# Kernel tuning notes

Measured on AMD Instinct MI355X. Metric: run time of the kernel, lower is better.

Reference implementation:

```python
import jax, jax.numpy as jnp
import numpy as np


def mp_conv1d(x, w, groups=1, pad=0):
    # EDM2-style magnitude-preserving conv: per-out-channel unit-norm weight, no bias.
    # effective w_hat = w / (eps + ||w||/sqrt(fan_in)) / sqrt(fan_in)  ~= w / ||w||
    fan_in = w.shape[1] * w.shape[2]
    norm = jnp.sqrt(jnp.sum(jnp.square(w), axis=(1, 2), keepdims=True))
    w_hat = w / ((1e-4 + norm / np.sqrt(fan_in)) * np.sqrt(fan_in))
    return jax.lax.conv_general_dilated(
        x, w_hat, window_strides=(1,), padding=[(pad, pad)],
        dimension_numbers=('NCH', 'OIH', 'NCH'), feature_group_count=groups)


def complex_log(x, eps=1e-6):
    real = jnp.log(jnp.maximum(jnp.abs(x), eps))
    imag = (x < 0).astype(real.dtype) * np.pi
    return jax.lax.complex(real, imag)


def logcumsumexp_complex(z, axis=-1):
    # parallel prefix logcumsumexp over complex values (stabilized by real part)
    def combine(a, b):
        m = jnp.maximum(a.real, b.real)
        m_safe = jnp.where(jnp.isfinite(m), m, 0.0)  # guard (-inf,-inf) pairs
        return m_safe + jnp.log(jnp.exp(a - m_safe) + jnp.exp(b - m_safe))
    return jax.lax.associative_scan(combine, z, axis=axis)


def log_parallel_scan(log_a, log_b, log_h0):
    # heinsen associative scan: h[t] = a[t]*h[t-1] + b[t], h[-1]=h0
    log_b = jnp.concatenate([log_h0[..., None].astype(log_b.dtype), log_b], axis=-1)
    pads = [(0, 0)] * (log_a.ndim - 1) + [(1, 0)]
    a_star = jnp.pad(jnp.cumsum(log_a, axis=-1), pads)  # [... L+1]
    log_h0_plus_b_star = logcumsumexp_complex(log_b - a_star, axis=-1)
    log_h = a_star + log_h0_plus_b_star
    return jnp.exp(log_h[..., 1:]).real


def min_gru(h, g):
    # o[t] = (1-sigmoid(g[t])) * o[t-1] + sigmoid(g[t]) * h[t], h0 = 0
    log_a = jax.nn.log_sigmoid(-g)
    log_b = jax.nn.log_sigmoid(g) + complex_log(h)
    log_h0 = jnp.full(h.shape[:-1], -jnp.inf, dtype=log_b.dtype)  # log(0)
    return log_parallel_scan(log_a, log_b, log_h0).astype(h.dtype)


def setup_inputs() -> dict:
    key = jax.random.key(0)
    k1, k2, k3, k4 = jax.random.split(key, 4)
    B, D, L, O = 4, 512, 8192, 512
    return {
        'x': jax.random.normal(k1, (B, D, L), jnp.float32),
        'conv_w': jax.random.normal(k2, (D, 1, 5), jnp.float32),
        'h_w': jax.random.normal(k3, (O, D, 1), jnp.float32),
        'g_w': jax.random.normal(k4, (O - 2, D, 1), jnp.float32),
    }


def reference(x, conv_w, h_w, g_w):
    c = mp_conv1d(x, conv_w, groups=x.shape[1], pad=2)  # depthwise 5-tap
    h = mp_conv1d(c, h_w)                               # [B O L]
    g = mp_conv1d(c, g_w)                               # [B O-2 L]
    B, _, L = g.shape
    g = jnp.concatenate([
        jnp.full((B, 1, L), -1000.0, g.dtype),
        jnp.full((B, 1, L), 1000.0, g.dtype),
        g], axis=1)                                     # polarize -> [B O L]
    return min_gru(h, g)
```

## Files before the change

### kernel.cpp

```cpp
#include <hip/hip_runtime.h>
#include <hip/hip_bf16.h>
#include <math.h>

typedef float f32x4 __attribute__((ext_vector_type(4)));
typedef short s16x8 __attribute__((ext_vector_type(8)));
typedef short s16x16 __attribute__((ext_vector_type(16)));

#define B_  4
#define D_  512
#define L_  8192
#define CH_ 512
#define M_  1024

typedef const __attribute__((address_space(1))) void g_cvoid;
typedef __attribute__((address_space(3))) void lds_void;

__device__ __forceinline__ unsigned short f2bf(float f) {
    union { float f; unsigned u; } v; v.f = f;
    unsigned r = v.u + 0x7FFFu + ((v.u >> 16) & 1u);
    return (unsigned short)(r >> 16);
}

__global__ __launch_bounds__(256)
void prep_kernel(const float* __restrict__ h_w, const float* __restrict__ g_w,
                 unsigned short* __restrict__ Wn) {
    __shared__ float red[4];
    const int ch = blockIdx.x, t = threadIdx.x;
    {
        float v0 = h_w[ch * 512 + t], v1 = h_w[ch * 512 + t + 256];
        float ss = v0 * v0 + v1 * v1;
        #pragma unroll
        for (int off = 32; off > 0; off >>= 1) ss += __shfl_down(ss, off, 64);
        if ((t & 63) == 0) red[t >> 6] = ss;
        __syncthreads();
        float tot = red[0] + red[1] + red[2] + red[3];
        float scale = 1.f / (sqrtf(tot) + 1e-4f * sqrtf(512.f));
        Wn[(size_t)(2 * ch) * 512 + t]       = f2bf(v0 * scale);
        Wn[(size_t)(2 * ch) * 512 + t + 256] = f2bf(v1 * scale);
    }
    __syncthreads();
    if (ch >= 2) {
        float v0 = g_w[(ch - 2) * 512 + t], v1 = g_w[(ch - 2) * 512 + t + 256];
        float ss = v0 * v0 + v1 * v1;
        #pragma unroll
        for (int off = 32; off > 0; off >>= 1) ss += __shfl_down(ss, off, 64);
        if ((t & 63) == 0) red[t >> 6] = ss;
        __syncthreads();
        float tot = red[0] + red[1] + red[2] + red[3];
        float scale = 1.f / (sqrtf(tot) + 1e-4f * sqrtf(512.f));
        Wn[(size_t)(2 * ch + 1) * 512 + t]       = f2bf(v0 * scale);
        Wn[(size_t)(2 * ch + 1) * 512 + t + 256] = f2bf(v1 * scale);
    } else {
        Wn[(size_t)(2 * ch + 1) * 512 + t]       = 0;
        Wn[(size_t)(2 * ch + 1) * 512 + t + 256] = 0;
    }
}

__global__ __launch_bounds__(512)
void w1n_kernel(const float* __restrict__ h_w, float* __restrict__ w1n_g) {
    __shared__ float red[8];
    const int t = threadIdx.x;
    const int sg = t >> 6;
    const int lane = t & 63;
    float v = h_w[512 + t];
    float ss = v * v;
    #pragma unroll
    for (int off = 32; off > 0; off >>= 1) ss += __shfl_down(ss, off, 64);
    if (lane == 0) red[sg] = ss;
    __syncthreads();
    float tot = ((red[0] + red[1]) + (red[2] + red[3]))
              + ((red[4] + red[5]) + (red[6] + red[7]));
    float sc = 1.f / (sqrtf(tot) + 1e-4f * sqrtf(512.f));
    w1n_g[t] = v * sc;
}

__global__ __launch_bounds__(256)
void convT_kernel(const float* __restrict__ x, const float* __restrict__ cw,
                  const float* __restrict__ w1n_g,
                  unsigned short* __restrict__ CT, float* __restrict__ Pp) {
    __shared__ float xs[64][72];
    __shared__ unsigned short ct[64][72];
    __shared__ float cvf[64][65];
    const int t = threadIdx.x;
    const int l0 = blockIdx.x * 64, d0 = blockIdx.y * 64, b = blockIdx.z;
    const int r = t >> 2, q = t & 3;
    const float* xr = x + (size_t)(b * 512 + d0 + r) * L_ + (l0 - 2);
    #pragma unroll
    for (int k = 0; k < 17; ++k) {
        int c = q + 4 * k;
        int lg = l0 - 2 + c;
        xs[r][c] = (lg >= 0 && lg < L_) ? xr[c] : 0.f;
    }
    float w0 = cw[(d0 + r) * 5 + 0], w1 = cw[(d0 + r) * 5 + 1],
          w2 = cw[(d0 + r) * 5 + 2], w3 = cw[(d0 + r) * 5 + 3],
          w4 = cw[(d0 + r) * 5 + 4];
    float ss = w0 * w0 + w1 * w1 + w2 * w2 + w3 * w3 + w4 * w4;
    float scale = 1.f / (sqrtf(ss) + 1e-4f * sqrtf(5.f));
    w0 *= scale; w1 *= scale; w2 *= scale; w3 *= scale; w4 *= scale;
    __syncthreads();
    #pragma unroll
    for (int k = 0; k < 16; ++k) {
        int li = q + 4 * k;
        float acc = w0 * xs[r][li + 0] + w1 * xs[r][li + 1] + w2 * xs[r][li + 2]
                  + w3 * xs[r][li + 3] + w4 * xs[r][li + 4];
        ct[li][r] = f2bf(acc);
        cvf[li][r] = acc;
    }
    __syncthreads();
    {
        int lr = t >> 2, seg = t & 3;
        s16x16 v = *(const s16x16*)&ct[lr][seg * 16];
        *(s16x16*)&CT[(size_t)(b * 8192 + l0 + lr) * 512 + d0 + seg * 16] = v;
    }
    if (t < 64) {
        float p = 0.f;
        for (int rr = 0; rr < 64; ++rr)
            p += w1n_g[d0 + rr] * cvf[t][rr];
        Pp[((size_t)blockIdx.y * B_ + b) * L_ + l0 + t] = p;
    }
}

__global__ __launch_bounds__(256)
void gemm_kernel(const unsigned short* __restrict__ Wn,
                 const unsigned short* __restrict__ CT,
                 unsigned* __restrict__ HG) {
    __shared__ unsigned short As[128 * 64];
    __shared__ unsigned short Bs[128 * 64];
    const int t = threadIdx.x;
    const int lane = t & 63, w = t >> 6;
    const int wgid = ((blockIdx.x & 7) << 8) | (blockIdx.x >> 3);
    const int mBase = (wgid & 7) * 128;
    const int nBase = (wgid >> 3) * 128;

    const int wrow = (w >> 1) * 64, wcol = (w & 1) * 64;

    const int srow_ = lane >> 3;
    const int schk  = (lane & 7) ^ srow_;

    f32x4 acc[4][4];
    #pragma unroll
    for (int fr = 0; fr < 4; ++fr)
        #pragma unroll
        for (int fc = 0; fc < 4; ++fc)
            acc[fr][fc] = (f32x4){0.f, 0.f, 0.f, 0.f};

    const unsigned short* gA = &Wn[(size_t)(mBase + w * 32 + srow_) * 512 + schk * 8];
    const unsigned short* gB = &CT[(size_t)(nBase + w * 32 + srow_) * 512 + schk * 8];

    const int g  = lane >> 4;
    const int c0 = ((0 + g) ^ (lane & 7)) * 8;
    const int c1 = ((4 + g) ^ (lane & 7)) * 8;

    #pragma unroll
    for (int ks = 0; ks < 8; ++ks) {
        const int k0 = ks * 64;
        #pragma unroll
        for (int i = 0; i < 4; ++i) {
            __builtin_amdgcn_global_load_lds(
                (g_cvoid*)(gA + (size_t)i * 8 * 512 + k0),
                (lds_void*)&As[(w * 32 + i * 8) * 64], 16, 0, 0);
            __builtin_amdgcn_global_load_lds(
                (g_cvoid*)(gB + (size_t)i * 8 * 512 + k0),
                (lds_void*)&Bs[(w * 32 + i * 8) * 64], 16, 0, 0);
        }
        __syncthreads();
        #pragma unroll
        for (int kh = 0; kh < 2; ++kh) {
            const int cc = (kh == 0) ? c0 : c1;
            s16x8 af[4], bf[4];
            #pragma unroll
            for (int f = 0; f < 4; ++f) {
                af[f] = *(const s16x8*)&As[(wrow + f * 16 + (lane & 15)) * 64 + cc];
                bf[f] = *(const s16x8*)&Bs[(wcol + f * 16 + (lane & 15)) * 64 + cc];
            }
            #pragma unroll
            for (int fr = 0; fr < 4; ++fr)
                #pragma unroll
                for (int fc = 0; fc < 4; ++fc)
                    acc[fr][fc] = __builtin_amdgcn_mfma_f32_16x16x32_bf16(
                        af[fr], bf[fc], acc[fr][fc], 0, 0, 0);
        }
        __syncthreads();
    }

    #pragma unroll
    for (int fr = 0; fr < 4; ++fr)
    #pragma unroll
    for (int fc = 0; fc < 4; ++fc) {
        f32x4 a = acc[fr][fc];
        const int gR0 = mBase + wrow + fr * 16 + ((lane >> 4) * 4);
        const int n   = nBase + wcol + fc * 16 + (lane & 15);
        const int bb  = n >> 13, l = n & 8191;
        #pragma unroll
        for (int p = 0; p < 2; ++p) {
            float hv = a[2 * p], gv = a[2 * p + 1];
            const int ch = (gR0 >> 1) + p;
            if (ch == 0)      gv = -1000.f;
            else if (ch == 1) gv =  1000.f;
            size_t off = ((size_t)bb * CH_ + ch) * L_ + l;
            HG[off] = ((unsigned)f2bf(hv) << 16) | (unsigned)f2bf(gv);
        }
    }
}

struct LV { float re, sg; };

__device__ __forceinline__ LV lcomb(LV a, LV b) {
    float m  = fmaxf(a.re, b.re);
    float ms = (m > -3.0e38f) ? m : 0.f;
    float s  = a.sg * __expf(a.re - ms) + b.sg * __expf(b.re - ms);
    LV r;
    r.re = ms + __logf(fabsf(s));
    r.sg = (s < 0.f) ? -1.f : 1.f;
    return r;
}

__global__ __launch_bounds__(512)
void logscan_kernel(const unsigned* __restrict__ HG,
                    const float* __restrict__ Pp,
                    float* __restrict__ Out) {
    __shared__ float wA[8];
    __shared__ float wRe[8], wSg[8];
    const int row = blockIdx.x;
    const int t = threadIdx.x;
    const int lane = t & 63, wid = t >> 6;
    const bool isCh1 = ((row & 511) == 1);
    const int bb = row >> 9;
    const unsigned* hp = HG + (size_t)row * L_;
    float* op = Out + (size_t)row * L_;

    float As[16], zz[16];
    unsigned sgb = 0;
    float run = 0.f;
    if (isCh1) {
        #pragma unroll
        for (int i = 0; i < 16; ++i) {
            const int l = t * 16 + i;
            float acc = Pp[((size_t)0 * B_ + bb) * L_ + l];
            #pragma unroll
            for (int gg = 1; gg < 8; ++gg)
                acc += Pp[((size_t)gg * B_ + bb) * L_ + l];
            if (acc < 0.f) sgb |= (1u << i);
            run -= 1000.f;
            As[i] = run;
            zz[i] = logf(fmaxf(fabsf(acc), 1e-6f));
        }
    } else {
        #pragma unroll
        for (int i = 0; i < 4; ++i) {
            uint4 h4 = *(const uint4*)&hp[t * 16 + i * 4];
            #pragma unroll
            for (int j = 0; j < 4; ++j) {
                int k = i * 4 + j;
                unsigned w32 = (j == 0) ? h4.x : (j == 1) ? h4.y
                             : (j == 2) ? h4.z : h4.w;
                float hv = __uint_as_float(w32 & 0xFFFF0000u);
                float gv = __uint_as_float(w32 << 16);
                float e  = __expf(-fabsf(gv));
                float l1 = __logf(1.f + e);
                float la = fminf(-gv, 0.f) - l1;
                float ls = fminf(gv, 0.f) - l1;
                if (hv < 0.f) sgb |= (1u << k);
                run += la;
                As[k] = run;
                zz[k] = ls + __logf(fmaxf(fabsf(hv), 1e-6f));
            }
        }
    }
    float wsc = run;
    #pragma unroll
    for (int off = 1; off < 64; off <<= 1) {
        float u = __shfl_up(wsc, off, 64);
        if (lane >= off) wsc += u;
    }
    if (lane == 63) wA[wid] = wsc;
    __syncthreads();
    float pre = wsc - run;
    for (int j = 0; j < wid; ++j) pre += wA[j];
    #pragma unroll
    for (int i = 0; i < 16; ++i) As[i] += pre;

    LV tot = { -INFINITY, 1.f };
    #pragma unroll
    for (int k = 0; k < 16; ++k) {
        zz[k] -= As[k];
        LV zi = { zz[k], ((sgb >> k) & 1) ? -1.f : 1.f };
        tot = lcomb(tot, zi);
    }
    LV sc = tot;
    #pragma unroll
    for (int off = 1; off < 64; off <<= 1) {
        float ure = __shfl_up(sc.re, off, 64);
        float usg = __shfl_up(sc.sg, off, 64);
        if (lane >= off) { LV u = { ure, usg }; sc = lcomb(u, sc); }
    }
    if (lane == 63) { wRe[wid] = sc.re; wSg[wid] = sc.sg; }
    __syncthreads();
    float pr = __shfl_up(sc.re, 1, 64);
    float ps = __shfl_up(sc.sg, 1, 64);
    LV lex = { -INFINITY, 1.f };
    if (lane != 0) { lex.re = pr; lex.sg = ps; }
    LV wpre = { -INFINITY, 1.f };
    for (int j = 0; j < wid; ++j) { LV u = { wRe[j], wSg[j] }; wpre = lcomb(wpre, u); }
    LV pref = lcomb(wpre, lex);

    LV run2 = pref;
    #pragma unroll
    for (int i = 0; i < 4; ++i) {
        float4 o4;
        #pragma unroll
        for (int j = 0; j < 4; ++j) {
            int k = i * 4 + j;
            LV zi = { zz[k], ((sgb >> k) & 1) ? -1.f : 1.f };
            run2 = lcomb(run2, zi);
            float ov = run2.sg * __expf(As[k] + run2.re);
            if (j == 0) o4.x = ov; else if (j == 1) o4.y = ov;
            else if (j == 2) o4.z = ov; else o4.w = ov;
        }
        *(float4*)&op[t * 16 + i * 4] = o4;
    }
}

extern "C" void kernel_launch(void* const* d_in, const int* in_sizes, int n_in,
                              void* d_out, int out_size, void* d_ws, size_t ws_size,
                              hipStream_t stream) {
    const float* x      = (const float*)d_in[0];
    const float* conv_w = (const float*)d_in[1];
    const float* h_w    = (const float*)d_in[2];
    const float* g_w    = (const float*)d_in[3];
    float* out = (float*)d_out;
    char* ws = (char*)d_ws;

    unsigned short* CT  = (unsigned short*)ws;
    unsigned short* Wn  = (unsigned short*)(ws + (size_t)32 * 1024 * 1024);
    unsigned*       HG  = (unsigned*)(ws + (size_t)33 * 1024 * 1024);
    const size_t base97 = (size_t)97 * 1024 * 1024;
    float* w1n_g = (float*)(ws + base97);
    float* Pp    = (float*)(ws + base97 + 16 * 1024);

    prep_kernel<<<512, 256, 0, stream>>>(h_w, g_w, Wn);
    w1n_kernel<<<1, 512, 0, stream>>>(h_w, w1n_g);
    convT_kernel<<<dim3(128, 8, 4), 256, 0, stream>>>(x, conv_w, w1n_g, CT, Pp);
    gemm_kernel<<<2048, 256, 0, stream>>>(Wn, CT, HG);
    logscan_kernel<<<B_ * CH_, 512, 0, stream>>>(HG, Pp, out);
}
```

Before: 149.5 us.

## Fuse log-sigmoid precompute into GEMM epilogue and simplify local log-scan

The GEMM epilogue now computes the log-sigmoid terms log_a and log_b directly and stores them as two fp16 values packed in one word, replacing the raw bf16 h/g pair. The sign of h is carried in the sign bit of the encoded log_a. The scan kernel therefore does no softplus or log work while loading. Its per-thread reduction and prefix pass also move from repeated pairwise log-add-exp combines to a running max and scaled sum, which removes most per-element log calls. The costs are extra transcendental work in the GEMM epilogue and some precision risk from fp16 storage. There is also an edge case: when log_a rounds to exactly +0, the sign encoding can mark the wrong sign of h.

```diff
diff --git a/kernel.cpp b/kernel.cpp
--- a/kernel.cpp
+++ b/kernel.cpp
@@ -1,5 +1,6 @@
 #include <hip/hip_runtime.h>
 #include <hip/hip_bf16.h>
+#include <hip/hip_fp16.h>
 #include <math.h>
 
 typedef float f32x4 __attribute__((ext_vector_type(4)));
@@ -197,8 +198,16 @@
             const int ch = (gR0 >> 1) + p;
             if (ch == 0)      gv = -1000.f;
             else if (ch == 1) gv =  1000.f;
+            float e  = __expf(-fabsf(gv));
+            float l1 = __logf(1.f + e);
+            float la = fminf(-gv, 0.f) - l1;
+            float ls = fminf(gv, 0.f) - l1;
+            float zb = ls + __logf(fmaxf(fabsf(hv), 1e-6f));
+            float enc = (hv < 0.f) ? -la : la;
+            unsigned short ula = __half_as_ushort(__float2half(enc));
+            unsigned short uzb = __half_as_ushort(__float2half(zb));
             size_t off = ((size_t)bb * CH_ + ch) * L_ + l;
-            HG[off] = ((unsigned)f2bf(hv) << 16) | (unsigned)f2bf(gv);
+            HG[off] = ((unsigned)uzb << 16) | (unsigned)ula;
         }
     }
 }
@@ -254,16 +263,14 @@
                 int k = i * 4 + j;
                 unsigned w32 = (j == 0) ? h4.x : (j == 1) ? h4.y
                              : (j == 2) ? h4.z : h4.w;
-                float hv = __uint_as_float(w32 & 0xFFFF0000u);
-                float gv = __uint_as_float(w32 << 16);
-                float e  = __expf(-fabsf(gv));
-                float l1 = __logf(1.f + e);
-                float la = fminf(-gv, 0.f) - l1;
-                float ls = fminf(gv, 0.f) - l1;
-                if (hv < 0.f) sgb |= (1u << k);
-                run += la;
+                unsigned short ula = (unsigned short)(w32 & 0xFFFFu);
+                unsigned short uzb = (unsigned short)(w32 >> 16);
+                float enc = __half2float(__ushort_as_half(ula));
+                float zbv = __half2float(__ushort_as_half(uzb));
+                if (!(ula >> 15)) sgb |= (1u << k);
+                run -= fabsf(enc);
                 As[k] = run;
-                zz[k] = ls + __logf(fmaxf(fabsf(hv), 1e-6f));
+                zz[k] = zbv;
             }
         }
     }
@@ -280,14 +287,20 @@
     #pragma unroll
     for (int i = 0; i < 16; ++i) As[i] += pre;
 
-    LV tot = { -INFINITY, 1.f };
+    float mstar = -INFINITY;
     #pragma unroll
     for (int k = 0; k < 16; ++k) {
         zz[k] -= As[k];
-        LV zi = { zz[k], ((sgb >> k) & 1) ? -1.f : 1.f };
-        tot = lcomb(tot, zi);
-    }
-    LV sc = tot;
+        mstar = fmaxf(mstar, zz[k]);
+    }
+    float ssum = 0.f;
+    #pragma unroll
+    for (int k = 0; k < 16; ++k)
+        ssum += (((sgb >> k) & 1) ? -1.f : 1.f) * __expf(zz[k] - mstar);
+    LV sc;
+    sc.re = mstar + __logf(fabsf(ssum));
+    sc.sg = (ssum < 0.f) ? -1.f : 1.f;
+
     #pragma unroll
     for (int off = 1; off < 64; off <<= 1) {
         float ure = __shfl_up(sc.re, off, 64);
@@ -304,16 +317,19 @@
     for (int j = 0; j < wid; ++j) { LV u = { wRe[j], wSg[j] }; wpre = lcomb(wpre, u); }
     LV pref = lcomb(wpre, lex);
 
-    LV run2 = pref;
+    float m2 = pref.re;
+    float s2 = pref.sg;
     #pragma unroll
     for (int i = 0; i < 4; ++i) {
         float4 o4;
         #pragma unroll
         for (int j = 0; j < 4; ++j) {
             int k = i * 4 + j;
-            LV zi = { zz[k], ((sgb >> k) & 1) ? -1.f : 1.f };
-            run2 = lcomb(run2, zi);
-            float ov = run2.sg * __expf(As[k] + run2.re);
+            float sk = ((sgb >> k) & 1) ? -1.f : 1.f;
+            float nm = fmaxf(m2, zz[k]);
+            s2 = s2 * __expf(m2 - nm) + sk * __expf(zz[k] - nm);
+            m2 = nm;
+            float ov = s2 * __expf(As[k] + m2);
             if (j == 0) o4.x = ov; else if (j == 1) o4.y = ov;
             else if (j == 2) o4.z = ov; else o4.w = ov;
         }
```

Measured after the change: 136.2 us. -8.9%, faster.
